# Kernel optimization log

Measured on AMD Instinct MI355X. Metric: run time of the kernel, lower is better.

The kernel has to match this reference:

```python
import jax, jax.numpy as jnp
import numpy as np


def setup_inputs() -> dict:
    key = jax.random.key(0)
    ks = jax.random.split(key, 7)
    b, h, w, c = 4, 64, 64, 256
    fc = 64
    s = 0.05  # small init so exp(-d^2) and softmax stay well-conditioned
    return {
        "feature_map": jax.random.normal(ks[0], (b, h, w, c), dtype=jnp.float32),
        "W_emb": jax.random.normal(ks[1], (fc, c), dtype=jnp.float32) * s,
        "b_emb": jax.random.normal(ks[2], (fc,), dtype=jnp.float32) * s,
        "W_att": jax.random.normal(ks[3], (c, c), dtype=jnp.float32) * s,
        "b_att": jax.random.normal(ks[4], (c,), dtype=jnp.float32) * s,
        "W_thr": jax.random.normal(ks[5], (1, c), dtype=jnp.float32) * s,
        "b_thr": jax.random.normal(ks[6], (1,), dtype=jnp.float32) * s,
        "layer": 0,
    }


def reference(feature_map, W_emb, b_emb, W_att, b_att, W_thr, b_thr, layer):
    # feature_map: (b, h, w, c) channels-last (torch permutes to NCHW; 1x1 convs
    # are pointwise matmuls, so we stay channels-last).
    b, h, w, c = feature_map.shape
    hw = h * w

    # embeddings_conv (1x1): (b,h,w,c) @ (c,fc) -> (b,hw,fc)
    emb = (jnp.einsum('bhwc,fc->bhwf', feature_map, W_emb) + b_emb).reshape(b, hw, -1)

    # ||ei - ej||^2 via expansion (avoids (b,hw,hw,fc) broadcast)
    sq_norm = jnp.sum(emb * emb, axis=-1)  # (b, hw)
    sq_dist = sq_norm[:, :, None] + sq_norm[:, None, :] - 2.0 * jnp.einsum('bif,bjf->bij', emb, emb)
    sq_dist = jnp.maximum(sq_dist, 0.0)
    sim = jnp.exp(-sq_dist)  # (b, hw, hw)

    # attention_conv (1x1)
    shortcut = jnp.einsum('bhwc,dc->bhwd', feature_map, W_att) + b_att  # (b,h,w,c)
    # instance_threshold_conv (1x1) on shortcut -> (b, hw)
    Tinst = (jnp.einsum('bhwc,oc->bhwo', shortcut, W_thr) + b_thr).reshape(b, hw)

    A = jnp.maximum(sim - Tinst[:, None, :], 0.0)
    A = jax.nn.softmax(A, axis=1)  # torch Softmax(dim=1) on (b, hw, hw)

    sc_flat = shortcut.reshape(b, hw, c)  # (b, hw, c)
    # torch: bmm(shortcut(b,c,hw), A^T) -> out[b,c,i] = sum_j sc[b,c,j] * A[b,i,j]
    inst = jnp.einsum('bjc,bij->bic', sc_flat, A).reshape(b, h, w, c)

    return feature_map + inst  # (b, h, w, c)
```

## Files before the change

kernel.cpp:

```cpp
#include <hip/hip_runtime.h>
#include <hip/hip_bf16.h>
#include <math.h>

typedef __attribute__((ext_vector_type(8))) short short8;
typedef __attribute__((ext_vector_type(4))) float f32x4;

#define BB 4
#define HW 4096
#define CC 256
#define FC 64
#define L2E 1.4426950408889634f

#define OFF_EMB   0
#define OFF_SCT2  (2*1024*1024)
#define OFF_SQN   (OFF_SCT2 + 8*1024*1024)
#define OFF_T     (OFF_SQN + 65536)
#define OFF_D     (OFF_T   + 65536)
#define OFF_WEMB2 (OFF_D   + 65536)
#define OFF_WATT2 (OFF_WEMB2 + 32768)

static __device__ __forceinline__ short f2bf(float f) {
    __hip_bfloat16 h = __float2bfloat16(f);
    return *reinterpret_cast<short*>(&h);
}
static __device__ __forceinline__ float bf2f(short s) {
    __hip_bfloat16 h = *reinterpret_cast<__hip_bfloat16*>(&s);
    return __bfloat162float(h);
}
static __device__ __forceinline__ float fexp2(float x) {
#if __has_builtin(__builtin_amdgcn_exp2f)
    return __builtin_amdgcn_exp2f(x);
#else
    float r; asm("v_exp_f32 %0, %1" : "=v"(r) : "v"(x)); return r;
#endif
}
static __device__ __forceinline__ float frcp(float x) {
#if __has_builtin(__builtin_amdgcn_rcpf)
    return __builtin_amdgcn_rcpf(x);
#else
    return 1.0f / x;
#endif
}

__global__ __launch_bounds__(256) void k_prep(const float* __restrict__ Wemb,
    const float* __restrict__ Watt, short* __restrict__ Wemb2,
    short* __restrict__ Watt2, float* __restrict__ D)
{
    const int bid = blockIdx.x, t = threadIdx.x;
    if (bid < 256) {
        Watt2[(size_t)(t>>3)*2048 + bid*8 + (t&7)] = f2bf(Watt[(size_t)bid*256 + t]);
        if (bid < 64) D[bid*256 + t] = 0.f;
    } else {
        const int f = bid - 256;
        Wemb2[(size_t)(t>>3)*512 + f*8 + (t&7)] = f2bf(Wemb[(size_t)f*256 + t]);
    }
}

__global__ __launch_bounds__(256) void k_front(const float* __restrict__ fm,
    const short* __restrict__ Wemb2, const short* __restrict__ Watt2,
    const float* __restrict__ bemb, const float* __restrict__ batt,
    const float* __restrict__ wthr, const float* __restrict__ bthr,
    short* __restrict__ emb, short* __restrict__ sct2,
    float* __restrict__ sqn, float* __restrict__ T)
{
    const int blk = blockIdx.x;
    const int b = blk >> 8;
    const int r0 = (blk & 255) * 16;
    const int t = threadIdx.x;
    const int w = t >> 6, lane = t & 63, g = lane >> 4, n16 = lane & 15;
    __shared__ short fmt[16*256];
    __shared__ float tred[16][4];
    __shared__ float qred[16][4];
    #pragma unroll
    for (int v = t; v < 512; v += 256) {
        const int row = v >> 5, c32 = v & 31;
        const float4* src = (const float4*)(fm + ((size_t)b*HW + r0 + row)*CC + c32*8);
        float4 x0 = src[0], x1 = src[1];
        short8 pv;
        pv[0]=f2bf(x0.x); pv[1]=f2bf(x0.y); pv[2]=f2bf(x0.z); pv[3]=f2bf(x0.w);
        pv[4]=f2bf(x1.x); pv[5]=f2bf(x1.y); pv[6]=f2bf(x1.z); pv[7]=f2bf(x1.w);
        *(short8*)((char*)fmt + row*512 + ((c32*16) ^ ((row&7)<<4))) = pv;
    }
    __syncthreads();
    const int cb = w*64, fb = w*16;
    f32x4 acc[4], acce;
    #pragma unroll
    for (int nn = 0; nn < 4; ++nn) acc[nn] = (f32x4){0.f,0.f,0.f,0.f};
    acce = (f32x4){0.f,0.f,0.f,0.f};
    #pragma unroll
    for (int kk = 0; kk < 8; ++kk) {
        const int kc = kk*4 + g;
        short8 a = *(const short8*)((const char*)fmt + n16*512 + ((kc*16) ^ ((n16&7)<<4)));
        const short* wb = Watt2 + (size_t)kc*2048 + (cb + n16)*8;
        #pragma unroll
        for (int nn = 0; nn < 4; ++nn) {
            short8 bv = *(const short8*)(wb + nn*128);
            acc[nn] = __builtin_amdgcn_mfma_f32_16x16x32_bf16(a, bv, acc[nn], 0, 0, 0);
        }
        short8 be = *(const short8*)(Wemb2 + (size_t)kc*512 + (fb + n16)*8);
        acce = __builtin_amdgcn_mfma_f32_16x16x32_bf16(a, be, acce, 0, 0, 0);
    }
    float tp[4] = {0.f,0.f,0.f,0.f};
    const int jt_ = r0 >> 6;
    const int jc0 = (r0 & 63) >> 3;
    const size_t tilebase = ((size_t)b*64 + jt_)*8;
    #pragma unroll
    for (int nn = 0; nn < 4; ++nn) {
        const int ch = cb + nn*16 + n16;
        const float ba_ = batt[ch], wt_ = wthr[ch];
        float v[4];
        #pragma unroll
        for (int r = 0; r < 4; ++r) { v[r] = acc[nn][r] + ba_; tp[r] = fmaf(v[r], wt_, tp[r]); }
        const int jc = jc0 + (g >> 1);
        const int jw0 = (g & 1)*4;
        short* dstp = sct2 + (tilebase + jc)*2048 + (size_t)ch*8;
        unsigned u01 = (unsigned short)f2bf(v[0]) | ((unsigned)(unsigned short)f2bf(v[1]) << 16);
        unsigned u23 = (unsigned short)f2bf(v[2]) | ((unsigned)(unsigned short)f2bf(v[3]) << 16);
        *(unsigned*)(dstp + jw0)     = u01;
        *(unsigned*)(dstp + jw0 + 2) = u23;
    }
    #pragma unroll
    for (int r = 0; r < 4; ++r)
        #pragma unroll
        for (int off = 1; off <= 8; off <<= 1) tp[r] += __shfl_xor(tp[r], off);
    const int f = fb + n16;
    const float be_ = bemb[f];
    float qp[4];
    #pragma unroll
    for (int r = 0; r < 4; ++r) {
        short bv = f2bf(acce[r] + be_);
        emb[((size_t)b*HW + r0 + g*4 + r)*FC + f] = bv;
        float ef = bf2f(bv);
        qp[r] = ef*ef;
        #pragma unroll
        for (int off = 1; off <= 8; off <<= 1) qp[r] += __shfl_xor(qp[r], off);
    }
    if (n16 == 0) {
        #pragma unroll
        for (int r = 0; r < 4; ++r) { tred[g*4+r][w] = tp[r]; qred[g*4+r][w] = qp[r]; }
    }
    __syncthreads();
    if (t < 16) {
        T[(size_t)b*HW + r0 + t]   = tred[t][0]+tred[t][1]+tred[t][2]+tred[t][3] + bthr[0];
        sqn[(size_t)b*HW + r0 + t] = qred[t][0]+qred[t][1]+qred[t][2]+qred[t][3];
    }
}

__global__ __launch_bounds__(256) void k_colsum(const short* __restrict__ emb,
    const float* __restrict__ sqn, const float* __restrict__ T,
    float* __restrict__ D)
{
    const int bid = blockIdx.x;
    const int split = bid & 7, jt = (bid >> 3) & 63, b = bid >> 9;
    const int t = threadIdx.x, w = t >> 6, lane = t & 63, g = lane >> 4, n16 = lane & 15;
    const size_t jbase = (size_t)b*HW + jt*64;
    __shared__ short ej[64*64];
    __shared__ short ei[2][64*64];
    __shared__ float sqni[2][64];
    #pragma unroll
    for (int v = t; v < 512; v += 256) {
        const int row = v >> 3, c8 = v & 7;
        short8 x = *(const short8*)(emb + (jbase + row)*FC + c8*8);
        *(short8*)((char*)ej + row*128 + ((c8*16) ^ ((row&7)<<4))) = x;
    }
    const int jl = w*16 + n16;
    const float sqjL = -L2E * sqn[jbase + jl];
    const float tjL  = -L2E * T[jbase + jl];
    const int srow0 = t >> 3, srow1 = (t >> 3) + 32, sc8 = t & 7;
    const int sb0 = srow0*128 + ((sc8*16) ^ ((srow0&7)<<4));
    const int sb1 = srow1*128 + ((sc8*16) ^ ((srow1&7)<<4));
    const size_t base0 = (size_t)b*HW + (size_t)split*512;
    short8 stg0 = *(const short8*)(emb + (base0 + srow0)*FC + sc8*8);
    short8 stg1 = *(const short8*)(emb + (base0 + srow1)*FC + sc8*8);
    float stgq = (t < 64) ? sqn[base0 + t] : 0.f;
    *(short8*)((char*)ei[0] + sb0) = stg0;
    *(short8*)((char*)ei[0] + sb1) = stg1;
    if (t < 64) sqni[0][t] = stgq;
    stg0 = *(const short8*)(emb + (base0 + 64 + srow0)*FC + sc8*8);
    stg1 = *(const short8*)(emb + (base0 + 64 + srow1)*FC + sc8*8);
    stgq = (t < 64) ? sqn[base0 + 64 + t] : 0.f;
    __syncthreads();
    const short8 bf0 = *(const short8*)((const char*)ej + jl*128 + ((g*16)     ^ ((jl&7)<<4)));
    const short8 bf1 = *(const short8*)((const char*)ej + jl*128 + (((g+4)*16) ^ ((jl&7)<<4)));
    float csum = 0.f;
    for (int it = 0; it < 8; ++it) {
        if (it < 7) {
            char* eib = (char*)ei[(it+1)&1];
            *(short8*)(eib + sb0) = stg0;
            *(short8*)(eib + sb1) = stg1;
            if (t < 64) sqni[(it+1)&1][t] = stgq;
            if (it < 6) {
                const size_t nb = base0 + (size_t)(it+2)*64;
                stg0 = *(const short8*)(emb + (nb + srow0)*FC + sc8*8);
                stg1 = *(const short8*)(emb + (nb + srow1)*FC + sc8*8);
                stgq = (t < 64) ? sqn[nb + t] : 0.f;
            }
        }
        const char* eib = (const char*)ei[it&1];
        const float* sqc = sqni[it&1];
        #pragma unroll
        for (int m = 0; m < 4; ++m) {
            const int arow = m*16 + n16;
            short8 a0 = *(const short8*)(eib + arow*128 + ((g*16)     ^ ((arow&7)<<4)));
            short8 a1 = *(const short8*)(eib + arow*128 + (((g+4)*16) ^ ((arow&7)<<4)));
            f32x4 dot = {0.f,0.f,0.f,0.f};
            dot = __builtin_amdgcn_mfma_f32_16x16x32_bf16(a0, bf0, dot, 0, 0, 0);
            dot = __builtin_amdgcn_mfma_f32_16x16x32_bf16(a1, bf1, dot, 0, 0, 0);
            #pragma unroll
            for (int r = 0; r < 4; ++r) {
                float x1 = fminf(fmaf(dot[r], 2.f*L2E, fmaf(-L2E, sqc[m*16 + g*4 + r], sqjL)), 0.f);
                float e1 = fexp2(x1);
                float a_ = fmaxf(fmaf(e1, L2E, tjL), 0.f);
                csum += fexp2(a_);
            }
        }
        __syncthreads();
    }
    csum += __shfl_xor(csum, 16);
    csum += __shfl_xor(csum, 32);
    if (lane < 16) atomicAdd(&D[jbase + jl], csum);
}

#define ATTN_ITER(K, bfC, sqC, tC, dC, bfN, sqN, tN, dN)                         \
  {                                                                              \
    const int kn = (K) < 63 ? (K) + 1 : 63;                                      \
    const size_t jbn = bbase + (size_t)kn * 64;                                  \
    sqN = sqn[jbn + jl]; tN = T[jbn + jl]; dN = D[jbn + jl];                     \
    {                                                                            \
      const short* sbn = sct2 + ((size_t)(b*64 + kn)*8)*2048 + (size_t)(w*32 + n16)*8; \
      _Pragma("unroll")                                                          \
      for (int nn = 0; nn < 2; ++nn) {                                           \
        _Pragma("unroll")                                                        \
        for (int kc = 0; kc < 2; ++kc)                                           \
          bfN[nn*2+kc] = *(const short8*)(sbn + (size_t)(kc*4+g)*2048 + nn*128); \
      }                                                                          \
    }                                                                            \
    {                                                                            \
      const float iD   = frcp(dC);                                               \
      const float sqjL = -L2E * sqC;                                             \
      const float tjL  = -L2E * tC;                                              \
      const char* ejb = (const char*)ejlds[(K)&1];                               \
      char* Pb = (char*)Plds[(K)&1];                                             \
      short8 b0 = *(const short8*)(ejb + jl*128 + ((g*16)     ^ ((jl&7)<<4)));   \
      short8 b1 = *(const short8*)(ejb + jl*128 + (((g+4)*16) ^ ((jl&7)<<4)));   \
      _Pragma("unroll")                                                          \
      for (int t2 = 0; t2 < 2; ++t2) {                                           \
        f32x4 dot = {0.f,0.f,0.f,0.f};                                           \
        dot = __builtin_amdgcn_mfma_f32_16x16x32_bf16(aQ0[t2], b0, dot, 0,0,0);  \
        dot = __builtin_amdgcn_mfma_f32_16x16x32_bf16(aQ1[t2], b1, dot, 0,0,0);  \
        _Pragma("unroll")                                                        \
        for (int r = 0; r < 4; ++r) {                                            \
          float x1 = fminf(fmaf(dot[r], 2.f*L2E, snL[t2][r] + sqjL), 0.f);       \
          float e1 = fexp2(x1);                                                  \
          float a_ = fmaxf(fmaf(e1, L2E, tjL), 0.f);                             \
          float p  = fexp2(a_) * iD;                                             \
          const int prow = ih*32 + t2*16 + g*4 + r;                              \
          *(short*)(Pb + prow*128 + (((jl>>3) ^ (prow&7))<<4) + (jl&7)*2) = f2bf(p); \
        }                                                                        \
      }                                                                          \
    }                                                                            \
    if ((K) < 63) {                                                              \
      *(short8*)((char*)ejlds[((K)+1)&1] + sbyte) = stg;                         \
      const int k2n = (K) < 62 ? (K) + 2 : 63;                                   \
      stg = *(const short8*)(emb + (bbase + (size_t)k2n*64 + srow)*FC + sc8*8);  \
    }                                                                            \
    __syncthreads();                                                             \
    {                                                                            \
      const char* Pb = (const char*)Plds[(K)&1];                                 \
      _Pragma("unroll")                                                          \
      for (int m = 0; m < 4; ++m) {                                              \
        const int prow = m*16 + n16;                                             \
        short8 pa0 = *(const short8*)(Pb + prow*128 + (((0*4+g)<<4) ^ ((prow&7)<<4))); \
        short8 pa1 = *(const short8*)(Pb + prow*128 + (((1*4+g)<<4) ^ ((prow&7)<<4))); \
        acc[m][0] = __builtin_amdgcn_mfma_f32_16x16x32_bf16(pa0, bfC[0], acc[m][0], 0,0,0); \
        acc[m][0] = __builtin_amdgcn_mfma_f32_16x16x32_bf16(pa1, bfC[1], acc[m][0], 0,0,0); \
        acc[m][1] = __builtin_amdgcn_mfma_f32_16x16x32_bf16(pa0, bfC[2], acc[m][1], 0,0,0); \
        acc[m][1] = __builtin_amdgcn_mfma_f32_16x16x32_bf16(pa1, bfC[3], acc[m][1], 0,0,0); \
      }                                                                          \
    }                                                                            \
  }

__global__ __launch_bounds__(512) void k_attn(const float* __restrict__ fm,
    const short* __restrict__ emb, const float* __restrict__ sqn,
    const float* __restrict__ T, const float* __restrict__ D,
    const short* __restrict__ sct2, float* __restrict__ out)
{
    const int bid = ((blockIdx.x & 7) << 5) | (blockIdx.x >> 3);
    const int b = bid >> 6;
    const int i0 = (bid & 63) * 64;
    const int t = threadIdx.x, w = t >> 6, lane = t & 63, g = lane >> 4, n16 = lane & 15;
    const size_t bbase = (size_t)b * HW;
    const size_t ibase = bbase + i0;
    __shared__ short ejlds[2][64*64];
    __shared__ short Plds[2][64*64];

    const int ih = w & 1, jq = w >> 1;
    const int jl = jq * 16 + n16;
    short8 aQ0[2], aQ1[2];
    float snL[2][4];
    #pragma unroll
    for (int t2 = 0; t2 < 2; ++t2) {
        const size_t qr = ibase + ih*32 + t2*16 + n16;
        aQ0[t2] = *(const short8*)(emb + qr*FC + g*8);
        aQ1[t2] = *(const short8*)(emb + qr*FC + 32 + g*8);
        #pragma unroll
        for (int r = 0; r < 4; ++r)
            snL[t2][r] = -L2E * sqn[ibase + ih*32 + t2*16 + g*4 + r];
    }
    const int srow = t >> 3, sc8 = t & 7;
    const int sbyte = srow*128 + ((sc8*16) ^ ((srow&7)<<4));
    short8 stg = *(const short8*)(emb + (bbase + srow)*FC + sc8*8);
    *(short8*)((char*)ejlds[0] + sbyte) = stg;
    stg = *(const short8*)(emb + (bbase + 64 + srow)*FC + sc8*8);
    float sqA = sqn[bbase + jl], tA = T[bbase + jl], dA = D[bbase + jl];
    float sqB, tB, dB;
    short8 bfA[4], bfB[4];
    {
        const short* sb0 = sct2 + ((size_t)(b*64)*8)*2048 + (size_t)(w*32 + n16)*8;
        #pragma unroll
        for (int nn = 0; nn < 2; ++nn)
            #pragma unroll
            for (int kc = 0; kc < 2; ++kc)
                bfA[nn*2+kc] = *(const short8*)(sb0 + (size_t)(kc*4+g)*2048 + nn*128);
    }
    f32x4 acc[4][2];
    #pragma unroll
    for (int m = 0; m < 4; ++m) { acc[m][0] = (f32x4){0.f,0.f,0.f,0.f}; acc[m][1] = (f32x4){0.f,0.f,0.f,0.f}; }
    __syncthreads();

    for (int k2 = 0; k2 < 64; k2 += 2) {
        ATTN_ITER(k2,   bfA, sqA, tA, dA, bfB, sqB, tB, dB);
        ATTN_ITER(k2+1, bfB, sqB, tB, dB, bfA, sqA, tA, dA);
    }

    #pragma unroll
    for (int m = 0; m < 4; ++m)
        #pragma unroll
        for (int r = 0; r < 4; ++r) {
            const size_t row = ibase + m*16 + g*4 + r;
            #pragma unroll
            for (int nn = 0; nn < 2; ++nn) {
                const size_t idx = row*CC + w*32 + nn*16 + n16;
                out[idx] = fm[idx] + acc[m][nn][r];
            }
        }
}

extern "C" void kernel_launch(void* const* d_in, const int* in_sizes, int n_in,
                              void* d_out, int out_size, void* d_ws, size_t ws_size,
                              hipStream_t stream)
{
    const float* fm   = (const float*)d_in[0];
    const float* Wemb = (const float*)d_in[1];
    const float* bemb = (const float*)d_in[2];
    const float* Watt = (const float*)d_in[3];
    const float* batt = (const float*)d_in[4];
    const float* Wthr = (const float*)d_in[5];
    const float* bthr = (const float*)d_in[6];
    char* ws = (char*)d_ws;
    short* emb   = (short*)(ws + OFF_EMB);
    short* sct2  = (short*)(ws + OFF_SCT2);
    float* sqn   = (float*)(ws + OFF_SQN);
    float* T     = (float*)(ws + OFF_T);
    float* D     = (float*)(ws + OFF_D);
    short* Wemb2 = (short*)(ws + OFF_WEMB2);
    short* Watt2 = (short*)(ws + OFF_WATT2);
    float* out = (float*)d_out;

    k_prep  <<<320,  256, 0, stream>>>(Wemb, Watt, Wemb2, Watt2, D);
    k_front <<<1024, 256, 0, stream>>>(fm, Wemb2, Watt2, bemb, batt, Wthr, bthr,
                                       emb, sct2, sqn, T);
    k_colsum<<<2048, 256, 0, stream>>>(emb, sqn, T, D);
    k_attn  <<<256,  512, 0, stream>>>(fm, emb, sqn, T, D, sct2, out);
}
```

Before: 102.9 us.

## Software-pipeline attention: overlap next tile's score/exp with current tile's PV MFMAs

```diff
diff --git a/kernel.cpp b/kernel.cpp
--- a/kernel.cpp
+++ b/kernel.cpp
@@ -3,6 +3,7 @@
 #include <math.h>
 
 typedef __attribute__((ext_vector_type(8))) short short8;
+typedef __attribute__((ext_vector_type(4))) short s16x4;
 typedef __attribute__((ext_vector_type(4))) float f32x4;
 
 #define BB 4
@@ -40,6 +41,13 @@
 #else
     return 1.0f / x;
 #endif
+}
+static __device__ __forceinline__ short xf1(float dot, float sq, float tt,
+                                            float id, float sni) {
+    float x1 = fminf(fmaf(dot, 2.f*L2E, fmaf(-L2E, sq, sni)), 0.f);
+    float e1 = fexp2(x1);
+    float a_ = fmaxf(fmaf(e1, L2E, -L2E*tt), 0.f);
+    return f2bf(fexp2(a_) * id);
 }
 
 __global__ __launch_bounds__(256) void k_prep(const float* __restrict__ Wemb,
@@ -221,63 +229,67 @@
     if (lane < 16) atomicAdd(&D[jbase + jl], csum);
 }
 
-#define ATTN_ITER(K, bfC, sqC, tC, dC, bfN, sqN, tN, dN)                         \
-  {                                                                              \
-    const int kn = (K) < 63 ? (K) + 1 : 63;                                      \
-    const size_t jbn = bbase + (size_t)kn * 64;                                  \
-    sqN = sqn[jbn + jl]; tN = T[jbn + jl]; dN = D[jbn + jl];                     \
-    {                                                                            \
-      const short* sbn = sct2 + ((size_t)(b*64 + kn)*8)*2048 + (size_t)(w*32 + n16)*8; \
-      _Pragma("unroll")                                                          \
-      for (int nn = 0; nn < 2; ++nn) {                                           \
-        _Pragma("unroll")                                                        \
-        for (int kc = 0; kc < 2; ++kc)                                           \
-          bfN[nn*2+kc] = *(const short8*)(sbn + (size_t)(kc*4+g)*2048 + nn*128); \
-      }                                                                          \
-    }                                                                            \
-    {                                                                            \
-      const float iD   = frcp(dC);                                               \
-      const float sqjL = -L2E * sqC;                                             \
-      const float tjL  = -L2E * tC;                                              \
-      const char* ejb = (const char*)ejlds[(K)&1];                               \
-      char* Pb = (char*)Plds[(K)&1];                                             \
-      short8 b0 = *(const short8*)(ejb + jl*128 + ((g*16)     ^ ((jl&7)<<4)));   \
-      short8 b1 = *(const short8*)(ejb + jl*128 + (((g+4)*16) ^ ((jl&7)<<4)));   \
-      _Pragma("unroll")                                                          \
-      for (int t2 = 0; t2 < 2; ++t2) {                                           \
-        f32x4 dot = {0.f,0.f,0.f,0.f};                                           \
-        dot = __builtin_amdgcn_mfma_f32_16x16x32_bf16(aQ0[t2], b0, dot, 0,0,0);  \
-        dot = __builtin_amdgcn_mfma_f32_16x16x32_bf16(aQ1[t2], b1, dot, 0,0,0);  \
-        _Pragma("unroll")                                                        \
-        for (int r = 0; r < 4; ++r) {                                            \
-          float x1 = fminf(fmaf(dot[r], 2.f*L2E, snL[t2][r] + sqjL), 0.f);       \
-          float e1 = fexp2(x1);                                                  \
-          float a_ = fmaxf(fmaf(e1, L2E, tjL), 0.f);                             \
-          float p  = fexp2(a_) * iD;                                             \
-          const int prow = ih*32 + t2*16 + g*4 + r;                              \
-          *(short*)(Pb + prow*128 + (((jl>>3) ^ (prow&7))<<4) + (jl&7)*2) = f2bf(p); \
-        }                                                                        \
-      }                                                                          \
-    }                                                                            \
-    if ((K) < 63) {                                                              \
-      *(short8*)((char*)ejlds[((K)+1)&1] + sbyte) = stg;                         \
-      const int k2n = (K) < 62 ? (K) + 2 : 63;                                   \
-      stg = *(const short8*)(emb + (bbase + (size_t)k2n*64 + srow)*FC + sc8*8);  \
-    }                                                                            \
-    __syncthreads();                                                             \
-    {                                                                            \
-      const char* Pb = (const char*)Plds[(K)&1];                                 \
-      _Pragma("unroll")                                                          \
-      for (int m = 0; m < 4; ++m) {                                              \
-        const int prow = m*16 + n16;                                             \
-        short8 pa0 = *(const short8*)(Pb + prow*128 + (((0*4+g)<<4) ^ ((prow&7)<<4))); \
-        short8 pa1 = *(const short8*)(Pb + prow*128 + (((1*4+g)<<4) ^ ((prow&7)<<4))); \
-        acc[m][0] = __builtin_amdgcn_mfma_f32_16x16x32_bf16(pa0, bfC[0], acc[m][0], 0,0,0); \
-        acc[m][0] = __builtin_amdgcn_mfma_f32_16x16x32_bf16(pa1, bfC[1], acc[m][0], 0,0,0); \
-        acc[m][1] = __builtin_amdgcn_mfma_f32_16x16x32_bf16(pa0, bfC[2], acc[m][1], 0,0,0); \
-        acc[m][1] = __builtin_amdgcn_mfma_f32_16x16x32_bf16(pa1, bfC[3], acc[m][1], 0,0,0); \
-      }                                                                          \
-    }                                                                            \
+#define PV2(PRr, BF, M0)                                                       \
+  { _Pragma("unroll")                                                          \
+    for (int m = M0; m < M0+2; ++m) {                                          \
+      const int prow = m*16 + n16;                                             \
+      short8 pa0 = *(const short8*)((PRr) + prow*128 + (((g)   ^ (prow&7))<<4)); \
+      short8 pa1 = *(const short8*)((PRr) + prow*128 + (((4+g) ^ (prow&7))<<4)); \
+      acc[m][0] = __builtin_amdgcn_mfma_f32_16x16x32_bf16(pa0, BF[0], acc[m][0], 0,0,0); \
+      acc[m][0] = __builtin_amdgcn_mfma_f32_16x16x32_bf16(pa1, BF[1], acc[m][0], 0,0,0); \
+      acc[m][1] = __builtin_amdgcn_mfma_f32_16x16x32_bf16(pa0, BF[2], acc[m][1], 0,0,0); \
+      acc[m][1] = __builtin_amdgcn_mfma_f32_16x16x32_bf16(pa1, BF[3], acc[m][1], 0,0,0); } }
+
+#define WINDOW(K, BFC, BFN, SQC, TC, DC, SQN_, TN_, DN_)                       \
+  {                                                                            \
+    const int kq2 = (K)+2 < 63 ? (K)+2 : 63;                                   \
+    { const size_t jb = bbase + (size_t)kq2*64 + jq*16 + g*4;                  \
+      SQN_ = *(const float4*)(sqn + jb); TN_ = *(const float4*)(T + jb);       \
+      DN_ = *(const float4*)(D + jb); }                                        \
+    { const int kb = (K)+1 < 63 ? (K)+1 : 63;                                  \
+      const short* sbn = sct2 + ((size_t)(b*64 + kb)*8)*2048 + (size_t)(w*32 + n16)*8; \
+      _Pragma("unroll")                                                        \
+      for (int nn = 0; nn < 2; ++nn)                                           \
+        _Pragma("unroll")                                                      \
+        for (int kc = 0; kc < 2; ++kc)                                         \
+          BFN[nn*2+kc] = *(const short8*)(sbn + (size_t)(kc*4+g)*2048 + nn*128); } \
+    const char* ejb = (const char*)ejlds[((K)+1)&1];                           \
+    char* Pw = (char*)Plds[((K)+1)&1];                                         \
+    const char* Pr = (const char*)Plds[(K)&1];                                 \
+    short8 aj0 = *(const short8*)(ejb + jl*128 + ((g*16) ^ ((jl&7)<<4)));      \
+    short8 aj1 = *(const short8*)(ejb + jl*128 + (((g+4)*16) ^ ((jl&7)<<4)));  \
+    f32x4 dot0 = {0.f,0.f,0.f,0.f}, dot1 = {0.f,0.f,0.f,0.f};                  \
+    dot0 = __builtin_amdgcn_mfma_f32_16x16x32_bf16(aj0, aQ00, dot0, 0,0,0);    \
+    dot0 = __builtin_amdgcn_mfma_f32_16x16x32_bf16(aj1, aQ10, dot0, 0,0,0);    \
+    dot1 = __builtin_amdgcn_mfma_f32_16x16x32_bf16(aj0, aQ01, dot1, 0,0,0);    \
+    dot1 = __builtin_amdgcn_mfma_f32_16x16x32_bf16(aj1, aQ11, dot1, 0,0,0);    \
+    if ((K) < 62) {                                                            \
+      *(short8*)((char*)ejlds[(K)&1] + sbyte) = stg;                           \
+      const int k3 = (K)+3 < 63 ? (K)+3 : 63;                                  \
+      stg = *(const short8*)(emb + (bbase + (size_t)k3*64 + srow)*FC + sc8*8); } \
+    float4 idq; idq.x = frcp(DC.x); idq.y = frcp(DC.y);                        \
+    idq.z = frcp(DC.z); idq.w = frcp(DC.w);                                    \
+    { s16x4 pk;                                                                \
+      pk[0] = xf1(dot0[0], SQC.x, TC.x, idq.x, sni0);                          \
+      pk[1] = xf1(dot0[1], SQC.y, TC.y, idq.y, sni0);                          \
+      pk[2] = xf1(dot0[2], SQC.z, TC.z, idq.z, sni0);                          \
+      pk[3] = xf1(dot0[3], SQC.w, TC.w, idq.w, sni0);                          \
+      const int prow = ihb + n16;                                              \
+      *(s16x4*)(Pw + prow*128 + ((pgr ^ (prow&7))<<4) + pofs) = pk; }          \
+    __builtin_amdgcn_s_setprio(1);                                             \
+    PV2(Pr, BFC, 0);                                                           \
+    __builtin_amdgcn_s_setprio(0);                                             \
+    { s16x4 pk;                                                                \
+      pk[0] = xf1(dot1[0], SQC.x, TC.x, idq.x, sni1);                          \
+      pk[1] = xf1(dot1[1], SQC.y, TC.y, idq.y, sni1);                          \
+      pk[2] = xf1(dot1[2], SQC.z, TC.z, idq.z, sni1);                          \
+      pk[3] = xf1(dot1[3], SQC.w, TC.w, idq.w, sni1);                          \
+      const int prow = ihb + 16 + n16;                                         \
+      *(s16x4*)(Pw + prow*128 + ((pgr ^ (prow&7))<<4) + pofs) = pk; }          \
+    __builtin_amdgcn_s_setprio(1);                                             \
+    PV2(Pr, BFC, 2);                                                           \
+    __builtin_amdgcn_s_setprio(0);                                             \
+    __syncthreads();                                                           \
   }
 
 __global__ __launch_bounds__(512) void k_attn(const float* __restrict__ fm,
@@ -295,42 +307,87 @@
     __shared__ short Plds[2][64*64];
 
     const int ih = w & 1, jq = w >> 1;
-    const int jl = jq * 16 + n16;
-    short8 aQ0[2], aQ1[2];
-    float snL[2][4];
-    #pragma unroll
-    for (int t2 = 0; t2 < 2; ++t2) {
-        const size_t qr = ibase + ih*32 + t2*16 + n16;
-        aQ0[t2] = *(const short8*)(emb + qr*FC + g*8);
-        aQ1[t2] = *(const short8*)(emb + qr*FC + 32 + g*8);
-        #pragma unroll
-        for (int r = 0; r < 4; ++r)
-            snL[t2][r] = -L2E * sqn[ibase + ih*32 + t2*16 + g*4 + r];
-    }
+    const int ihb = ih * 32;
+    const int jl = jq*16 + n16;
+    const int pgr = jq*2 + (g>>1), pofs = (g&1)*8;
+
+    const short8 aQ00 = *(const short8*)(emb + (ibase + ihb      + n16)*FC + g*8);
+    const short8 aQ10 = *(const short8*)(emb + (ibase + ihb      + n16)*FC + g*8 + 32);
+    const short8 aQ01 = *(const short8*)(emb + (ibase + ihb + 16 + n16)*FC + g*8);
+    const short8 aQ11 = *(const short8*)(emb + (ibase + ihb + 16 + n16)*FC + g*8 + 32);
+    const float sni0 = -L2E * sqn[ibase + ihb + n16];
+    const float sni1 = -L2E * sqn[ibase + ihb + 16 + n16];
+
     const int srow = t >> 3, sc8 = t & 7;
     const int sbyte = srow*128 + ((sc8*16) ^ ((srow&7)<<4));
-    short8 stg = *(const short8*)(emb + (bbase + srow)*FC + sc8*8);
-    *(short8*)((char*)ejlds[0] + sbyte) = stg;
-    stg = *(const short8*)(emb + (bbase + 64 + srow)*FC + sc8*8);
-    float sqA = sqn[bbase + jl], tA = T[bbase + jl], dA = D[bbase + jl];
-    float sqB, tB, dB;
-    short8 bfA[4], bfB[4];
-    {
-        const short* sb0 = sct2 + ((size_t)(b*64)*8)*2048 + (size_t)(w*32 + n16)*8;
-        #pragma unroll
-        for (int nn = 0; nn < 2; ++nn)
-            #pragma unroll
-            for (int kc = 0; kc < 2; ++kc)
-                bfA[nn*2+kc] = *(const short8*)(sb0 + (size_t)(kc*4+g)*2048 + nn*128);
-    }
+    short8 e0 = *(const short8*)(emb + (bbase + srow)*FC + sc8*8);
+    *(short8*)((char*)ejlds[0] + sbyte) = e0;
+    short8 stg = *(const short8*)(emb + (bbase + 64 + srow)*FC + sc8*8);
+
+    const size_t jb0 = bbase + jq*16 + g*4;
+    const float4 SQ0 = *(const float4*)(sqn + jb0);
+    const float4 T0q = *(const float4*)(T + jb0);
+    const float4 D0q = *(const float4*)(D + jb0);
+    float4 SQA, TA, DA, SQB, TB, DB;
+    { const size_t jb = bbase + 64 + jq*16 + g*4;
+      SQA = *(const float4*)(sqn + jb); TA = *(const float4*)(T + jb);
+      DA = *(const float4*)(D + jb); }
+    short8 BFA[4], BFB[4];
+    { const short* sb0 = sct2 + ((size_t)(b*64)*8)*2048 + (size_t)(w*32 + n16)*8;
+      #pragma unroll
+      for (int nn = 0; nn < 2; ++nn)
+          #pragma unroll
+          for (int kc = 0; kc < 2; ++kc)
+              BFA[nn*2+kc] = *(const short8*)(sb0 + (size_t)(kc*4+g)*2048 + nn*128); }
+
     f32x4 acc[4][2];
     #pragma unroll
     for (int m = 0; m < 4; ++m) { acc[m][0] = (f32x4){0.f,0.f,0.f,0.f}; acc[m][1] = (f32x4){0.f,0.f,0.f,0.f}; }
     __syncthreads();
 
-    for (int k2 = 0; k2 < 64; k2 += 2) {
-        ATTN_ITER(k2,   bfA, sqA, tA, dA, bfB, sqB, tB, dB);
-        ATTN_ITER(k2+1, bfB, sqB, tB, dB, bfA, sqA, tA, dA);
+    {
+        const char* ejb = (const char*)ejlds[0];
+        char* Pw = (char*)Plds[0];
+        short8 aj0 = *(const short8*)(ejb + jl*128 + ((g*16) ^ ((jl&7)<<4)));
+        short8 aj1 = *(const short8*)(ejb + jl*128 + (((g+4)*16) ^ ((jl&7)<<4)));
+        f32x4 dot0 = {0.f,0.f,0.f,0.f}, dot1 = {0.f,0.f,0.f,0.f};
+        dot0 = __builtin_amdgcn_mfma_f32_16x16x32_bf16(aj0, aQ00, dot0, 0,0,0);
+        dot0 = __builtin_amdgcn_mfma_f32_16x16x32_bf16(aj1, aQ10, dot0, 0,0,0);
+        dot1 = __builtin_amdgcn_mfma_f32_16x16x32_bf16(aj0, aQ01, dot1, 0,0,0);
+        dot1 = __builtin_amdgcn_mfma_f32_16x16x32_bf16(aj1, aQ11, dot1, 0,0,0);
+        *(short8*)((char*)ejlds[1] + sbyte) = stg;
+        stg = *(const short8*)(emb + (bbase + 128 + srow)*FC + sc8*8);
+        float4 idq; idq.x = frcp(D0q.x); idq.y = frcp(D0q.y);
+        idq.z = frcp(D0q.z); idq.w = frcp(D0q.w);
+        { s16x4 pk;
+          pk[0] = xf1(dot0[0], SQ0.x, T0q.x, idq.x, sni0);
+          pk[1] = xf1(dot0[1], SQ0.y, T0q.y, idq.y, sni0);
+          pk[2] = xf1(dot0[2], SQ0.z, T0q.z, idq.z, sni0);
+          pk[3] = xf1(dot0[3], SQ0.w, T0q.w, idq.w, sni0);
+          const int prow = ihb + n16;
+          *(s16x4*)(Pw + prow*128 + ((pgr ^ (prow&7))<<4) + pofs) = pk; }
+        { s16x4 pk;
+          pk[0] = xf1(dot1[0], SQ0.x, T0q.x, idq.x, sni1);
+          pk[1] = xf1(dot1[1], SQ0.y, T0q.y, idq.y, sni1);
+          pk[2] = xf1(dot1[2], SQ0.z, T0q.z, idq.z, sni1);
+          pk[3] = xf1(dot1[3], SQ0.w, T0q.w, idq.w, sni1);
+          const int prow = ihb + 16 + n16;
+          *(s16x4*)(Pw + prow*128 + ((pgr ^ (prow&7))<<4) + pofs) = pk; }
+        __syncthreads();
+    }
+
+    for (int k2 = 0; k2 < 62; k2 += 2) {
+        WINDOW(k2,   BFA, BFB, SQA, TA, DA, SQB, TB, DB);
+        WINDOW(k2+1, BFB, BFA, SQB, TB, DB, SQA, TA, DA);
+    }
+    WINDOW(62, BFA, BFB, SQA, TA, DA, SQB, TB, DB);
+
+    {
+        const char* Pr = (const char*)Plds[1];
+        __builtin_amdgcn_s_setprio(1);
+        PV2(Pr, BFB, 0);
+        PV2(Pr, BFB, 2);
+        __builtin_amdgcn_s_setprio(0);
     }
 
     #pragma unroll
```

Measured after the change: 113.4 us. 1.1x slower.

## Retile attention kernel to 32-row blocks with prologue-skewed P/PV pipeline

Applied to the files above, without the earlier changes.

```diff
diff --git a/kernel.cpp b/kernel.cpp
--- a/kernel.cpp
+++ b/kernel.cpp
@@ -3,6 +3,7 @@
 #include <math.h>
 
 typedef __attribute__((ext_vector_type(8))) short short8;
+typedef __attribute__((ext_vector_type(4))) short s16x4;
 typedef __attribute__((ext_vector_type(4))) float f32x4;
 
 #define BB 4
@@ -40,6 +41,13 @@
 #else
     return 1.0f / x;
 #endif
+}
+static __device__ __forceinline__ short xf1(float dot, float sq, float tt,
+                                            float id, float sni) {
+    float x1 = fminf(fmaf(dot, 2.f*L2E, fmaf(-L2E, sq, sni)), 0.f);
+    float e1 = fexp2(x1);
+    float a_ = fmaxf(fmaf(e1, L2E, -L2E*tt), 0.f);
+    return f2bf(fexp2(a_) * id);
 }
 
 __global__ __launch_bounds__(256) void k_prep(const float* __restrict__ Wemb,
@@ -227,9 +235,9 @@
     const size_t jbn = bbase + (size_t)kn * 64;                                  \
     sqN = sqn[jbn + jl]; tN = T[jbn + jl]; dN = D[jbn + jl];                     \
     {                                                                            \
-      const short* sbn = sct2 + ((size_t)(b*64 + kn)*8)*2048 + (size_t)(w*32 + n16)*8; \
+      const short* sbn = sct2 + ((size_t)(b*64 + kn)*8)*2048 + (size_t)(w*64 + n16)*8; \
       _Pragma("unroll")                                                          \
-      for (int nn = 0; nn < 2; ++nn) {                                           \
+      for (int nn = 0; nn < 4; ++nn) {                                           \
         _Pragma("unroll")                                                        \
         for (int kc = 0; kc < 2; ++kc)                                           \
           bfN[nn*2+kc] = *(const short8*)(sbn + (size_t)(kc*4+g)*2048 + nn*128); \
@@ -254,93 +262,150 @@
           float e1 = fexp2(x1);                                                  \
           float a_ = fmaxf(fmaf(e1, L2E, tjL), 0.f);                             \
           float p  = fexp2(a_) * iD;                                             \
-          const int prow = ih*32 + t2*16 + g*4 + r;                              \
+          const int prow = t2*16 + g*4 + r;                                      \
           *(short*)(Pb + prow*128 + (((jl>>3) ^ (prow&7))<<4) + (jl&7)*2) = f2bf(p); \
         }                                                                        \
       }                                                                          \
     }                                                                            \
     if ((K) < 63) {                                                              \
-      *(short8*)((char*)ejlds[((K)+1)&1] + sbyte) = stg;                         \
+      *(short8*)((char*)ejlds[((K)+1)&1] + sbyte0) = stg0;                       \
+      *(short8*)((char*)ejlds[((K)+1)&1] + sbyte1) = stg1;                       \
       const int k2n = (K) < 62 ? (K) + 2 : 63;                                   \
-      stg = *(const short8*)(emb + (bbase + (size_t)k2n*64 + srow)*FC + sc8*8);  \
+      stg0 = *(const short8*)(emb + (bbase + (size_t)k2n*64 + srow0)*FC + sc8*8); \
+      stg1 = *(const short8*)(emb + (bbase + (size_t)k2n*64 + srow1)*FC + sc8*8); \
     }                                                                            \
     __syncthreads();                                                             \
     {                                                                            \
       const char* Pb = (const char*)Plds[(K)&1];                                 \
       _Pragma("unroll")                                                          \
-      for (int m = 0; m < 4; ++m) {                                              \
+      for (int m = 0; m < 2; ++m) {                                              \
         const int prow = m*16 + n16;                                             \
         short8 pa0 = *(const short8*)(Pb + prow*128 + (((0*4+g)<<4) ^ ((prow&7)<<4))); \
         short8 pa1 = *(const short8*)(Pb + prow*128 + (((1*4+g)<<4) ^ ((prow&7)<<4))); \
-        acc[m][0] = __builtin_amdgcn_mfma_f32_16x16x32_bf16(pa0, bfC[0], acc[m][0], 0,0,0); \
-        acc[m][0] = __builtin_amdgcn_mfma_f32_16x16x32_bf16(pa1, bfC[1], acc[m][0], 0,0,0); \
-        acc[m][1] = __builtin_amdgcn_mfma_f32_16x16x32_bf16(pa0, bfC[2], acc[m][1], 0,0,0); \
-        acc[m][1] = __builtin_amdgcn_mfma_f32_16x16x32_bf16(pa1, bfC[3], acc[m][1], 0,0,0); \
+        _Pragma("unroll")                                                        \
+        for (int nn = 0; nn < 4; ++nn) {                                         \
+          acc[m][nn] = __builtin_amdgcn_mfma_f32_16x16x32_bf16(pa0, bfC[nn*2+0], acc[m][nn], 0,0,0); \
+          acc[m][nn] = __builtin_amdgcn_mfma_f32_16x16x32_bf16(pa1, bfC[nn*2+1], acc[m][nn], 0,0,0); \
+        }                                                                        \
       }                                                                          \
     }                                                                            \
   }
 
-__global__ __launch_bounds__(512) void k_attn(const float* __restrict__ fm,
+__global__ __launch_bounds__(256, 2) void k_attn(const float* __restrict__ fm,
     const short* __restrict__ emb, const float* __restrict__ sqn,
     const float* __restrict__ T, const float* __restrict__ D,
     const short* __restrict__ sct2, float* __restrict__ out)
 {
-    const int bid = ((blockIdx.x & 7) << 5) | (blockIdx.x >> 3);
-    const int b = bid >> 6;
-    const int i0 = (bid & 63) * 64;
+    const int bid = ((blockIdx.x & 7) << 6) | (blockIdx.x >> 3);
+    const int b = bid >> 7;
+    const int i0 = (bid & 127) * 32;
     const int t = threadIdx.x, w = t >> 6, lane = t & 63, g = lane >> 4, n16 = lane & 15;
     const size_t bbase = (size_t)b * HW;
     const size_t ibase = bbase + i0;
     __shared__ short ejlds[2][64*64];
-    __shared__ short Plds[2][64*64];
-
-    const int ih = w & 1, jq = w >> 1;
-    const int jl = jq * 16 + n16;
+    __shared__ short Plds[2][32*64];
+
+    const int jl = w*16 + n16;
+
     short8 aQ0[2], aQ1[2];
     float snL[2][4];
     #pragma unroll
     for (int t2 = 0; t2 < 2; ++t2) {
-        const size_t qr = ibase + ih*32 + t2*16 + n16;
+        const size_t qr = ibase + t2*16 + n16;
         aQ0[t2] = *(const short8*)(emb + qr*FC + g*8);
         aQ1[t2] = *(const short8*)(emb + qr*FC + 32 + g*8);
         #pragma unroll
         for (int r = 0; r < 4; ++r)
-            snL[t2][r] = -L2E * sqn[ibase + ih*32 + t2*16 + g*4 + r];
-    }
-    const int srow = t >> 3, sc8 = t & 7;
-    const int sbyte = srow*128 + ((sc8*16) ^ ((srow&7)<<4));
-    short8 stg = *(const short8*)(emb + (bbase + srow)*FC + sc8*8);
-    *(short8*)((char*)ejlds[0] + sbyte) = stg;
-    stg = *(const short8*)(emb + (bbase + 64 + srow)*FC + sc8*8);
-    float sqA = sqn[bbase + jl], tA = T[bbase + jl], dA = D[bbase + jl];
-    float sqB, tB, dB;
-    short8 bfA[4], bfB[4];
+            snL[t2][r] = -L2E * sqn[ibase + t2*16 + g*4 + r];
+    }
+    const int srow0 = t >> 3, srow1 = (t >> 3) + 32, sc8 = t & 7;
+    const int sbyte0 = srow0*128 + ((sc8*16) ^ ((srow0&7)<<4));
+    const int sbyte1 = srow1*128 + ((sc8*16) ^ ((srow1&7)<<4));
+    short8 stg0 = *(const short8*)(emb + (bbase + srow0)*FC + sc8*8);
+    short8 stg1 = *(const short8*)(emb + (bbase + srow1)*FC + sc8*8);
+    *(short8*)((char*)ejlds[0] + sbyte0) = stg0;
+    *(short8*)((char*)ejlds[0] + sbyte1) = stg1;
+    stg0 = *(const short8*)(emb + (bbase + 64 + srow0)*FC + sc8*8);
+    stg1 = *(const short8*)(emb + (bbase + 64 + srow1)*FC + sc8*8);
+
+    const float sq0 = sqn[bbase + jl], t0q = T[bbase + jl], d0q = D[bbase + jl];
+    float sqA, tA, dA, sqB, tB, dB;
+    sqA = sqn[bbase + 64 + jl]; tA = T[bbase + 64 + jl]; dA = D[bbase + 64 + jl];
+    short8 bfA[8], bfB[8];
     {
-        const short* sb0 = sct2 + ((size_t)(b*64)*8)*2048 + (size_t)(w*32 + n16)*8;
-        #pragma unroll
-        for (int nn = 0; nn < 2; ++nn)
+        const short* sb0 = sct2 + ((size_t)(b*64)*8)*2048 + (size_t)(w*64 + n16)*8;
+        #pragma unroll
+        for (int nn = 0; nn < 4; ++nn)
             #pragma unroll
             for (int kc = 0; kc < 2; ++kc)
                 bfA[nn*2+kc] = *(const short8*)(sb0 + (size_t)(kc*4+g)*2048 + nn*128);
     }
-    f32x4 acc[4][2];
-    #pragma unroll
-    for (int m = 0; m < 4; ++m) { acc[m][0] = (f32x4){0.f,0.f,0.f,0.f}; acc[m][1] = (f32x4){0.f,0.f,0.f,0.f}; }
+    f32x4 acc[2][4];
+    #pragma unroll
+    for (int m = 0; m < 2; ++m)
+        #pragma unroll
+        for (int nn = 0; nn < 4; ++nn) acc[m][nn] = (f32x4){0.f,0.f,0.f,0.f};
     __syncthreads();
 
-    for (int k2 = 0; k2 < 64; k2 += 2) {
+    {
+        const char* ejb = (const char*)ejlds[0];
+        char* Pb = (char*)Plds[0];
+        const float iD = frcp(d0q);
+        const float sqjL = -L2E * sq0;
+        const float tjL  = -L2E * t0q;
+        short8 b0 = *(const short8*)(ejb + jl*128 + ((g*16)     ^ ((jl&7)<<4)));
+        short8 b1 = *(const short8*)(ejb + jl*128 + (((g+4)*16) ^ ((jl&7)<<4)));
+        #pragma unroll
+        for (int t2 = 0; t2 < 2; ++t2) {
+            f32x4 dot = {0.f,0.f,0.f,0.f};
+            dot = __builtin_amdgcn_mfma_f32_16x16x32_bf16(aQ0[t2], b0, dot, 0,0,0);
+            dot = __builtin_amdgcn_mfma_f32_16x16x32_bf16(aQ1[t2], b1, dot, 0,0,0);
+            #pragma unroll
+            for (int r = 0; r < 4; ++r) {
+                float x1 = fminf(fmaf(dot[r], 2.f*L2E, snL[t2][r] + sqjL), 0.f);
+                float e1 = fexp2(x1);
+                float a_ = fmaxf(fmaf(e1, L2E, tjL), 0.f);
+                float p  = fexp2(a_) * iD;
+                const int prow = t2*16 + g*4 + r;
+                *(short*)(Pb + prow*128 + (((jl>>3) ^ (prow&7))<<4) + (jl&7)*2) = f2bf(p);
+            }
+        }
+        *(short8*)((char*)ejlds[1] + sbyte0) = stg0;
+        *(short8*)((char*)ejlds[1] + sbyte1) = stg1;
+        stg0 = *(const short8*)(emb + (bbase + 128 + srow0)*FC + sc8*8);
+        stg1 = *(const short8*)(emb + (bbase + 128 + srow1)*FC + sc8*8);
+        __syncthreads();
+    }
+
+    for (int k2 = 0; k2 < 62; k2 += 2) {
         ATTN_ITER(k2,   bfA, sqA, tA, dA, bfB, sqB, tB, dB);
         ATTN_ITER(k2+1, bfB, sqB, tB, dB, bfA, sqA, tA, dA);
     }
-
-    #pragma unroll
-    for (int m = 0; m < 4; ++m)
+    ATTN_ITER(62, bfA, sqA, tA, dA, bfB, sqB, tB, dB);
+
+    {
+        const char* Pb = (const char*)Plds[1];
+        #pragma unroll
+        for (int m = 0; m < 2; ++m) {
+            const int prow = m*16 + n16;
+            short8 pa0 = *(const short8*)(Pb + prow*128 + (((0*4+g)<<4) ^ ((prow&7)<<4)));
+            short8 pa1 = *(const short8*)(Pb + prow*128 + (((1*4+g)<<4) ^ ((prow&7)<<4)));
+            #pragma unroll
+            for (int nn = 0; nn < 4; ++nn) {
+                acc[m][nn] = __builtin_amdgcn_mfma_f32_16x16x32_bf16(pa0, bfB[nn*2+0], acc[m][nn], 0,0,0);
+                acc[m][nn] = __builtin_amdgcn_mfma_f32_16x16x32_bf16(pa1, bfB[nn*2+1], acc[m][nn], 0,0,0);
+            }
+        }
+    }
+
+    #pragma unroll
+    for (int m = 0; m < 2; ++m)
         #pragma unroll
         for (int r = 0; r < 4; ++r) {
             const size_t row = ibase + m*16 + g*4 + r;
             #pragma unroll
-            for (int nn = 0; nn < 2; ++nn) {
-                const size_t idx = row*CC + w*32 + nn*16 + n16;
+            for (int nn = 0; nn < 4; ++nn) {
+                const size_t idx = row*CC + w*64 + nn*16 + n16;
                 out[idx] = fm[idx] + acc[m][nn][r];
             }
         }
@@ -371,5 +436,5 @@
     k_front <<<1024, 256, 0, stream>>>(fm, Wemb2, Watt2, bemb, batt, Wthr, bthr,
                                        emb, sct2, sqn, T);
     k_colsum<<<2048, 256, 0, stream>>>(emb, sqn, T, D);
-    k_attn  <<<256,  512, 0, stream>>>(fm, emb, sqn, T, D, sct2, out);
-}
+    k_attn  <<<512,  256, 0, stream>>>(fm, emb, sqn, T, D, sct2, out);
+}
```

Measured after the change: 111.2 us. 1.08x slower.

## Process two key tiles per barrier window in attention kernel

Applied to the files above, without the earlier changes.

```diff
diff --git a/kernel.cpp b/kernel.cpp
--- a/kernel.cpp
+++ b/kernel.cpp
@@ -41,6 +41,7 @@
     return 1.0f / x;
 #endif
 }
+#define MFMA32(a, b, c) __builtin_amdgcn_mfma_f32_16x16x32_bf16(a, b, c, 0, 0, 0)
 
 __global__ __launch_bounds__(256) void k_prep(const float* __restrict__ Wemb,
     const float* __restrict__ Watt, short* __restrict__ Wemb2,
@@ -95,10 +96,10 @@
         #pragma unroll
         for (int nn = 0; nn < 4; ++nn) {
             short8 bv = *(const short8*)(wb + nn*128);
-            acc[nn] = __builtin_amdgcn_mfma_f32_16x16x32_bf16(a, bv, acc[nn], 0, 0, 0);
+            acc[nn] = MFMA32(a, bv, acc[nn]);
         }
         short8 be = *(const short8*)(Wemb2 + (size_t)kc*512 + (fb + n16)*8);
-        acce = __builtin_amdgcn_mfma_f32_16x16x32_bf16(a, be, acce, 0, 0, 0);
+        acce = MFMA32(a, be, acce);
     }
     float tp[4] = {0.f,0.f,0.f,0.f};
     const int jt_ = r0 >> 6;
@@ -204,8 +205,8 @@
             short8 a0 = *(const short8*)(eib + arow*128 + ((g*16)     ^ ((arow&7)<<4)));
             short8 a1 = *(const short8*)(eib + arow*128 + (((g+4)*16) ^ ((arow&7)<<4)));
             f32x4 dot = {0.f,0.f,0.f,0.f};
-            dot = __builtin_amdgcn_mfma_f32_16x16x32_bf16(a0, bf0, dot, 0, 0, 0);
-            dot = __builtin_amdgcn_mfma_f32_16x16x32_bf16(a1, bf1, dot, 0, 0, 0);
+            dot = MFMA32(a0, bf0, dot);
+            dot = MFMA32(a1, bf1, dot);
             #pragma unroll
             for (int r = 0; r < 4; ++r) {
                 float x1 = fminf(fmaf(dot[r], 2.f*L2E, fmaf(-L2E, sqc[m*16 + g*4 + r], sqjL)), 0.f);
@@ -221,66 +222,89 @@
     if (lane < 16) atomicAdd(&D[jbase + jl], csum);
 }
 
-#define ATTN_ITER(K, bfC, sqC, tC, dC, bfN, sqN, tN, dN)                         \
-  {                                                                              \
-    const int kn = (K) < 63 ? (K) + 1 : 63;                                      \
-    const size_t jbn = bbase + (size_t)kn * 64;                                  \
-    sqN = sqn[jbn + jl]; tN = T[jbn + jl]; dN = D[jbn + jl];                     \
-    {                                                                            \
-      const short* sbn = sct2 + ((size_t)(b*64 + kn)*8)*2048 + (size_t)(w*32 + n16)*8; \
-      _Pragma("unroll")                                                          \
-      for (int nn = 0; nn < 2; ++nn) {                                           \
-        _Pragma("unroll")                                                        \
-        for (int kc = 0; kc < 2; ++kc)                                           \
-          bfN[nn*2+kc] = *(const short8*)(sbn + (size_t)(kc*4+g)*2048 + nn*128); \
-      }                                                                          \
-    }                                                                            \
-    {                                                                            \
-      const float iD   = frcp(dC);                                               \
-      const float sqjL = -L2E * sqC;                                             \
-      const float tjL  = -L2E * tC;                                              \
-      const char* ejb = (const char*)ejlds[(K)&1];                               \
-      char* Pb = (char*)Plds[(K)&1];                                             \
-      short8 b0 = *(const short8*)(ejb + jl*128 + ((g*16)     ^ ((jl&7)<<4)));   \
-      short8 b1 = *(const short8*)(ejb + jl*128 + (((g+4)*16) ^ ((jl&7)<<4)));   \
-      _Pragma("unroll")                                                          \
-      for (int t2 = 0; t2 < 2; ++t2) {                                           \
-        f32x4 dot = {0.f,0.f,0.f,0.f};                                           \
-        dot = __builtin_amdgcn_mfma_f32_16x16x32_bf16(aQ0[t2], b0, dot, 0,0,0);  \
-        dot = __builtin_amdgcn_mfma_f32_16x16x32_bf16(aQ1[t2], b1, dot, 0,0,0);  \
-        _Pragma("unroll")                                                        \
-        for (int r = 0; r < 4; ++r) {                                            \
-          float x1 = fminf(fmaf(dot[r], 2.f*L2E, snL[t2][r] + sqjL), 0.f);       \
-          float e1 = fexp2(x1);                                                  \
-          float a_ = fmaxf(fmaf(e1, L2E, tjL), 0.f);                             \
-          float p  = fexp2(a_) * iD;                                             \
-          const int prow = ih*32 + t2*16 + g*4 + r;                              \
-          *(short*)(Pb + prow*128 + (((jl>>3) ^ (prow&7))<<4) + (jl&7)*2) = f2bf(p); \
-        }                                                                        \
-      }                                                                          \
-    }                                                                            \
-    if ((K) < 63) {                                                              \
-      *(short8*)((char*)ejlds[((K)+1)&1] + sbyte) = stg;                         \
-      const int k2n = (K) < 62 ? (K) + 2 : 63;                                   \
-      stg = *(const short8*)(emb + (bbase + (size_t)k2n*64 + srow)*FC + sc8*8);  \
-    }                                                                            \
-    __syncthreads();                                                             \
-    {                                                                            \
-      const char* Pb = (const char*)Plds[(K)&1];                                 \
-      _Pragma("unroll")                                                          \
-      for (int m = 0; m < 4; ++m) {                                              \
-        const int prow = m*16 + n16;                                             \
-        short8 pa0 = *(const short8*)(Pb + prow*128 + (((0*4+g)<<4) ^ ((prow&7)<<4))); \
-        short8 pa1 = *(const short8*)(Pb + prow*128 + (((1*4+g)<<4) ^ ((prow&7)<<4))); \
-        acc[m][0] = __builtin_amdgcn_mfma_f32_16x16x32_bf16(pa0, bfC[0], acc[m][0], 0,0,0); \
-        acc[m][0] = __builtin_amdgcn_mfma_f32_16x16x32_bf16(pa1, bfC[1], acc[m][0], 0,0,0); \
-        acc[m][1] = __builtin_amdgcn_mfma_f32_16x16x32_bf16(pa0, bfC[2], acc[m][1], 0,0,0); \
-        acc[m][1] = __builtin_amdgcn_mfma_f32_16x16x32_bf16(pa1, bfC[3], acc[m][1], 0,0,0); \
-      }                                                                          \
-    }                                                                            \
+#define SCORE_XF(TT, EJB, PW, SQ, TJ, DD)                                      \
+  {                                                                            \
+    const char* ejb_ = (EJB) + (TT)*8192;                                      \
+    short8 b0 = *(const short8*)(ejb_ + jl*128 + ((g*16)     ^ ((jl&7)<<4)));  \
+    short8 b1 = *(const short8*)(ejb_ + jl*128 + (((g+4)*16) ^ ((jl&7)<<4)));  \
+    const float iD   = frcp(DD);                                               \
+    const float sqjL = -L2E * (SQ);                                            \
+    const float tjL  = -L2E * (TJ);                                            \
+    _Pragma("unroll")                                                          \
+    for (int t2 = 0; t2 < 2; ++t2) {                                           \
+      f32x4 dot = {0.f,0.f,0.f,0.f};                                           \
+      dot = MFMA32(aQ0[t2], b0, dot);                                          \
+      dot = MFMA32(aQ1[t2], b1, dot);                                          \
+      _Pragma("unroll")                                                        \
+      for (int r = 0; r < 4; ++r) {                                            \
+        float x1 = fminf(fmaf(dot[r], 2.f*L2E, snL[t2][r] + sqjL), 0.f);       \
+        float a_ = fmaxf(fmaf(fexp2(x1), L2E, tjL), 0.f);                      \
+        const int prow = ih*32 + t2*16 + g*4 + r;                              \
+        *(short*)((PW) + (TT)*8192 + prow*128                                  \
+                  + (((jl>>3) ^ (prow&7))<<4) + (jl&7)*2)                      \
+            = f2bf(fexp2(a_) * iD);                                            \
+      }                                                                        \
+    }                                                                          \
   }
 
-__global__ __launch_bounds__(512) void k_attn(const float* __restrict__ fm,
+#define PV_TILE(TT, PB, BF)                                                    \
+  { _Pragma("unroll")                                                          \
+    for (int m = 0; m < 4; ++m) {                                              \
+      const int prow = m*16 + n16;                                             \
+      short8 pa0 = *(const short8*)((PB) + (TT)*8192 + prow*128                \
+                                    + (((0*4+g) ^ (prow&7))<<4));              \
+      short8 pa1 = *(const short8*)((PB) + (TT)*8192 + prow*128                \
+                                    + (((1*4+g) ^ (prow&7))<<4));              \
+      _Pragma("unroll")                                                        \
+      for (int nn = 0; nn < 2; ++nn) {                                         \
+        acc[m][nn] = MFMA32(pa0, (BF)[nn*2+0], acc[m][nn]);                    \
+        acc[m][nn] = MFMA32(pa1, (BF)[nn*2+1], acc[m][nn]);                    \
+      }                                                                        \
+    } }
+
+#define LOAD_BF(DST, TILE)                                                     \
+  { const short* sb_ = sct2 + ((size_t)(b*64 + (TILE))*8)*2048                 \
+                            + (size_t)(w*32 + n16)*8;                          \
+    _Pragma("unroll")                                                          \
+    for (int nn = 0; nn < 2; ++nn)                                             \
+      _Pragma("unroll")                                                        \
+      for (int kc = 0; kc < 2; ++kc)                                           \
+        (DST)[nn*2+kc] = *(const short8*)(sb_ + (size_t)(kc*4+g)*2048 + nn*128); }
+
+#define WIN(W, q0C,t0C,d0C, q1C,t1C,d1C, bf0C,bf1C,                            \
+            q0N,t0N,d0N, q1N,t1N,d1N, bf0N,bf1N)                               \
+  {                                                                            \
+    const int k0n = (2*(W)+2 < 64) ? 2*(W)+2 : 63;                             \
+    const int k1n = (2*(W)+3 < 64) ? 2*(W)+3 : 63;                             \
+    q0N = sqn[bbase + (size_t)k0n*64 + jl];                                    \
+    t0N = T  [bbase + (size_t)k0n*64 + jl];                                    \
+    d0N = D  [bbase + (size_t)k0n*64 + jl];                                    \
+    q1N = sqn[bbase + (size_t)k1n*64 + jl];                                    \
+    t1N = T  [bbase + (size_t)k1n*64 + jl];                                    \
+    d1N = D  [bbase + (size_t)k1n*64 + jl];                                    \
+    LOAD_BF(bf0N, k0n)                                                         \
+    LOAD_BF(bf1N, k1n)                                                         \
+    const char* Eb = (const char*)ejlds[(W)&1];                                \
+    char* Pw = (char*)Plds[(W)&1];                                             \
+    SCORE_XF(0, Eb, Pw, q0C, t0C, d0C)                                         \
+    SCORE_XF(1, Eb, Pw, q1C, t1C, d1C)                                         \
+    { char* En = (char*)ejlds[((W)+1)&1];                                      \
+      *(short8*)(En + sbyte) = stgA;                                           \
+      *(short8*)(En + 8192 + sbyte) = stgB;                                    \
+      const int k0s = (2*(W)+4 < 64) ? 2*(W)+4 : 63;                           \
+      const int k1s = (2*(W)+5 < 64) ? 2*(W)+5 : 63;                           \
+      stgA = *(const short8*)(emb + (bbase + (size_t)k0s*64 + srow)*FC + sc8*8); \
+      stgB = *(const short8*)(emb + (bbase + (size_t)k1s*64 + srow)*FC + sc8*8); \
+    }                                                                          \
+    __syncthreads();                                                           \
+    const char* Pb = (const char*)Plds[(W)&1];                                 \
+    __builtin_amdgcn_s_setprio(1);                                             \
+    PV_TILE(0, Pb, bf0C)                                                       \
+    PV_TILE(1, Pb, bf1C)                                                       \
+    __builtin_amdgcn_s_setprio(0);                                             \
+  }
+
+__global__ __launch_bounds__(512, 2) void k_attn(const float* __restrict__ fm,
     const short* __restrict__ emb, const float* __restrict__ sqn,
     const float* __restrict__ T, const float* __restrict__ D,
     const short* __restrict__ sct2, float* __restrict__ out)
@@ -291,11 +315,12 @@
     const int t = threadIdx.x, w = t >> 6, lane = t & 63, g = lane >> 4, n16 = lane & 15;
     const size_t bbase = (size_t)b * HW;
     const size_t ibase = bbase + i0;
-    __shared__ short ejlds[2][64*64];
-    __shared__ short Plds[2][64*64];
+    __shared__ short ejlds[2][2*64*64];
+    __shared__ short Plds[2][2*64*64];
 
     const int ih = w & 1, jq = w >> 1;
-    const int jl = jq * 16 + n16;
+    const int jl = jq*16 + n16;
+
     short8 aQ0[2], aQ1[2];
     float snL[2][4];
     #pragma unroll
@@ -309,28 +334,32 @@
     }
     const int srow = t >> 3, sc8 = t & 7;
     const int sbyte = srow*128 + ((sc8*16) ^ ((srow&7)<<4));
-    short8 stg = *(const short8*)(emb + (bbase + srow)*FC + sc8*8);
-    *(short8*)((char*)ejlds[0] + sbyte) = stg;
-    stg = *(const short8*)(emb + (bbase + 64 + srow)*FC + sc8*8);
-    float sqA = sqn[bbase + jl], tA = T[bbase + jl], dA = D[bbase + jl];
-    float sqB, tB, dB;
-    short8 bfA[4], bfB[4];
-    {
-        const short* sb0 = sct2 + ((size_t)(b*64)*8)*2048 + (size_t)(w*32 + n16)*8;
-        #pragma unroll
-        for (int nn = 0; nn < 2; ++nn)
-            #pragma unroll
-            for (int kc = 0; kc < 2; ++kc)
-                bfA[nn*2+kc] = *(const short8*)(sb0 + (size_t)(kc*4+g)*2048 + nn*128);
-    }
+
+    short8 stgA = *(const short8*)(emb + (bbase + srow)*FC + sc8*8);
+    short8 stgB = *(const short8*)(emb + (bbase + 64 + srow)*FC + sc8*8);
+    *(short8*)((char*)ejlds[0] + sbyte) = stgA;
+    *(short8*)((char*)ejlds[0] + 8192 + sbyte) = stgB;
+    stgA = *(const short8*)(emb + (bbase + 128 + srow)*FC + sc8*8);
+    stgB = *(const short8*)(emb + (bbase + 192 + srow)*FC + sc8*8);
+    float q0A = sqn[bbase + jl],      t0A = T[bbase + jl],      d0A = D[bbase + jl];
+    float q1A = sqn[bbase + 64 + jl], t1A = T[bbase + 64 + jl], d1A = D[bbase + 64 + jl];
+    float q0B, t0B, d0B, q1B, t1B, d1B;
+    short8 bf0A[4], bf1A[4], bf0B[4], bf1B[4];
+    LOAD_BF(bf0A, 0)
+    LOAD_BF(bf1A, 1)
     f32x4 acc[4][2];
     #pragma unroll
-    for (int m = 0; m < 4; ++m) { acc[m][0] = (f32x4){0.f,0.f,0.f,0.f}; acc[m][1] = (f32x4){0.f,0.f,0.f,0.f}; }
+    for (int m = 0; m < 4; ++m) {
+        acc[m][0] = (f32x4){0.f,0.f,0.f,0.f};
+        acc[m][1] = (f32x4){0.f,0.f,0.f,0.f};
+    }
     __syncthreads();
 
-    for (int k2 = 0; k2 < 64; k2 += 2) {
-        ATTN_ITER(k2,   bfA, sqA, tA, dA, bfB, sqB, tB, dB);
-        ATTN_ITER(k2+1, bfB, sqB, tB, dB, bfA, sqA, tA, dA);
+    for (int w2 = 0; w2 < 32; w2 += 2) {
+        WIN(w2,   q0A,t0A,d0A, q1A,t1A,d1A, bf0A,bf1A,
+                  q0B,t0B,d0B, q1B,t1B,d1B, bf0B,bf1B)
+        WIN(w2+1, q0B,t0B,d0B, q1B,t1B,d1B, bf0B,bf1B,
+                  q0A,t0A,d0A, q1A,t1A,d1A, bf0A,bf1A)
     }
 
     #pragma unroll
```

Result: slower. 106.7 us (+3.6%).
